# Kernel tuning notes

Measured on AMD Instinct MI355X. Metric: run time of the kernel, lower is better.

## Reference

```python
import jax, jax.numpy as jnp
import numpy as np

N_NODES = 10000
N_EDGES = 320000
HIDDEN = 16
LABELS = 7


def setup_inputs() -> dict:
    key = jax.random.key(0)
    k1, k2, k3, k4, k5 = jax.random.split(key, 5)
    features = jax.random.normal(k1, (N_NODES, N_NODES), dtype=jnp.float32)
    src = jax.random.randint(k2, (N_EDGES,), 0, N_NODES, dtype=jnp.int64)
    dst = jax.random.randint(k3, (N_EDGES,), 0, N_NODES, dtype=jnp.int64)
    # Glorot-ish params as in DGL GraphConv
    W1 = jax.random.normal(k4, (N_NODES, HIDDEN), dtype=jnp.float32) * (1.0 / np.sqrt(N_NODES))
    b1 = jnp.zeros((HIDDEN,), dtype=jnp.float32)
    W2 = jax.random.normal(k5, (HIDDEN, LABELS), dtype=jnp.float32) * (1.0 / np.sqrt(HIDDEN))
    b2 = jnp.zeros((LABELS,), dtype=jnp.float32)
    return {"features": features, "src": src, "dst": dst,
            "W1": W1, "b1": b1, "W2": W2, "b2": b2}


def reference(features, src, dst, W1, b1, W2, b2):
    N = features.shape[0]
    ones = jnp.ones(src.shape[0], dtype=features.dtype)
    out_deg = jnp.clip(jax.ops.segment_sum(ones, src, num_segments=N), 1.0)
    in_deg = jnp.clip(jax.ops.segment_sum(ones, dst, num_segments=N), 1.0)
    norm_src = jax.lax.rsqrt(out_deg)[:, None]  # D_out^{-1/2}
    norm_dst = jax.lax.rsqrt(in_deg)[:, None]   # D_in^{-1/2}

    def gconv(h, W, b):
        # DGL GraphConv norm='both'; in_feats >= out_feats so W applied first
        h = (h * norm_src) @ W                       # [N, out]
        agg = jax.ops.segment_sum(h[src], dst, num_segments=N)
        return agg * norm_dst + b

    h = jax.nn.relu(gconv(features, W1, b1))  # relu(relu(.)) == relu(.)
    return gconv(h, W2, b2)
```

## Files before the change

kernel.cpp:

```cpp
#include <hip/hip_runtime.h>


constexpr int NN  = 10000;
constexpr int NE  = 320000;
constexpr int HID = 16;
constexpr int LAB = 7;
constexpr int CAP = 128;

__global__ void k_count_fill(const int* __restrict__ src, const int* __restrict__ dst,
                             int* __restrict__ cnt_out, int* __restrict__ cnt_in,
                             int* __restrict__ esrc) {
  const int e = blockIdx.x * blockDim.x + threadIdx.x;
  if (e < NE) {
    const int s = src[e], d = dst[e];
    atomicAdd(&cnt_out[s], 1);
    const int p = atomicAdd(&cnt_in[d], 1);
    if (p < CAP) esrc[(d << 7) + p] = s;
  }
}

__global__ __launch_bounds__(256) void k_gemm1(const float* __restrict__ F,
                                               const float* __restrict__ W1,
                                               const int* __restrict__ cnt_out,
                                               float* __restrict__ Y1a,
                                               float* __restrict__ Y1b) {
  constexpr int BJ = 500;
  constexpr int TILES = 10;
  __shared__ float wT[HID * BJ];
  const int tid  = threadIdx.x;
  const int lane = tid & 63;
  const int wave = tid >> 6;
  const int row0 = blockIdx.x * 16 + wave * 4;
  const int jbase = blockIdx.y * 5000;
  float* __restrict__ Yout = blockIdx.y ? Y1b : Y1a;

  float acc[4][HID];
  #pragma unroll
  for (int m = 0; m < 4; ++m)
    #pragma unroll
    for (int k = 0; k < HID; ++k) acc[m][k] = 0.0f;

  for (int t = 0; t < TILES; ++t) {
    const int jt = jbase + t * BJ;
    __syncthreads();
    for (int u = tid; u < BJ * 4; u += 256) {
      const int j = u >> 2, k4 = u & 3;
      const float4 v = *(const float4*)(W1 + (size_t)(jt + j) * HID + k4 * 4);
      wT[(k4 * 4 + 0) * BJ + j] = v.x;
      wT[(k4 * 4 + 1) * BJ + j] = v.y;
      wT[(k4 * 4 + 2) * BJ + j] = v.z;
      wT[(k4 * 4 + 3) * BJ + j] = v.w;
    }
    __syncthreads();

    const float* Fr = F + (size_t)row0 * NN + jt;
    #pragma unroll
    for (int c = 0; c < 2; ++c) {
      const int j4 = lane + 64 * c;
      if (j4 < BJ / 4) {
        const int j = j4 * 4;
        const float4 f0 = *(const float4*)(Fr + j);
        const float4 f1 = *(const float4*)(Fr + NN + j);
        const float4 f2 = *(const float4*)(Fr + 2 * NN + j);
        const float4 f3 = *(const float4*)(Fr + 3 * NN + j);
        #pragma unroll
        for (int k = 0; k < HID; ++k) {
          const float4 w = *(const float4*)(wT + k * BJ + j);
          acc[0][k] = fmaf(f0.x, w.x, fmaf(f0.y, w.y, fmaf(f0.z, w.z, fmaf(f0.w, w.w, acc[0][k]))));
          acc[1][k] = fmaf(f1.x, w.x, fmaf(f1.y, w.y, fmaf(f1.z, w.z, fmaf(f1.w, w.w, acc[1][k]))));
          acc[2][k] = fmaf(f2.x, w.x, fmaf(f2.y, w.y, fmaf(f2.z, w.z, fmaf(f2.w, w.w, acc[2][k]))));
          acc[3][k] = fmaf(f3.x, w.x, fmaf(f3.y, w.y, fmaf(f3.z, w.z, fmaf(f3.w, w.w, acc[3][k]))));
        }
      }
    }
  }

  #pragma unroll
  for (int m = 0; m < 4; ++m)
    #pragma unroll
    for (int k = 0; k < HID; ++k) {
      float v = acc[m][k];
      #pragma unroll
      for (int off = 32; off > 0; off >>= 1) v += __shfl_down(v, off, 64);
      acc[m][k] = v;
    }

  if (lane == 0) {
    #pragma unroll
    for (int m = 0; m < 4; ++m) {
      const int row = row0 + m;
      const float s = rsqrtf(fmaxf((float)cnt_out[row], 1.0f));
      float4 o0 = {acc[m][0] * s, acc[m][1] * s, acc[m][2] * s, acc[m][3] * s};
      float4 o1 = {acc[m][4] * s, acc[m][5] * s, acc[m][6] * s, acc[m][7] * s};
      float4 o2 = {acc[m][8] * s, acc[m][9] * s, acc[m][10] * s, acc[m][11] * s};
      float4 o3 = {acc[m][12] * s, acc[m][13] * s, acc[m][14] * s, acc[m][15] * s};
      float4* yp = (float4*)(Yout + (size_t)row * HID);
      yp[0] = o0; yp[1] = o1; yp[2] = o2; yp[3] = o3;
    }
  }
}

__global__ __launch_bounds__(256) void k_gather1(
    const int* __restrict__ cnt_out, const int* __restrict__ cnt_in,
    const int* __restrict__ esrc,
    const float* __restrict__ Y1a, const float* __restrict__ Y1b,
    const float* __restrict__ b1, const float* __restrict__ W2,
    float* __restrict__ H2) {
  __shared__ float hsh[4][16];
  const int tid = threadIdx.x, lane = tid & 63, wave = tid >> 6;
  const int i = blockIdx.x * 4 + wave;
  const int n = min(cnt_in[i], CAP);
  const int* el = esrc + ((size_t)i << 7);
  const int sub = lane >> 4, k = lane & 15;
  float sum = 0.0f;
  for (int e = sub; e < n; e += 4) {
    const int s = el[e];
    sum += Y1a[s * HID + k] + Y1b[s * HID + k];
  }
  sum += __shfl_down(sum, 32, 64);
  sum += __shfl_down(sum, 16, 64);
  if (lane < 16) {
    const float ndv = rsqrtf(fmaxf((float)n, 1.0f));
    hsh[wave][k] = fmaxf(fmaf(sum, ndv, b1[k]), 0.0f);
  }
  __syncthreads();
  if (lane < 8) {
    float z = 0.0f;
    if (lane < LAB) {
      #pragma unroll
      for (int kk = 0; kk < HID; ++kk)
        z = fmaf(hsh[wave][kk], W2[kk * LAB + lane], z);
      z *= rsqrtf(fmaxf((float)cnt_out[i], 1.0f));
    }
    H2[i * 8 + lane] = z;
  }
}

__global__ __launch_bounds__(256) void k_gather2(
    const int* __restrict__ cnt_in, const int* __restrict__ esrc,
    const float* __restrict__ H2, const float* __restrict__ b2,
    float* __restrict__ out) {
  const int tid = threadIdx.x, lane = tid & 63, wave = tid >> 6;
  const int i = blockIdx.x * 4 + wave;
  const int n = min(cnt_in[i], CAP);
  const int* el = esrc + ((size_t)i << 7);
  const int sub = lane >> 3, c = lane & 7;
  float sum = 0.0f;
  for (int e = sub; e < n; e += 8) {
    sum += H2[(el[e] << 3) + c];
  }
  sum += __shfl_down(sum, 32, 64);
  sum += __shfl_down(sum, 16, 64);
  sum += __shfl_down(sum, 8, 64);
  if (lane < LAB) {
    const float ndv = rsqrtf(fmaxf((float)n, 1.0f));
    out[i * LAB + lane] = fmaf(sum, ndv, b2[lane]);
  }
}

extern "C" void kernel_launch(void* const* d_in, const int* in_sizes, int n_in,
                              void* d_out, int out_size, void* d_ws, size_t ws_size,
                              hipStream_t stream) {
  const float* F   = (const float*)d_in[0];
  const int*   src = (const int*)d_in[1];
  const int*   dst = (const int*)d_in[2];
  const float* W1  = (const float*)d_in[3];
  const float* b1  = (const float*)d_in[4];
  const float* W2  = (const float*)d_in[5];
  const float* b2  = (const float*)d_in[6];
  float* out = (float*)d_out;

  int* cnt_out = (int*)d_ws;
  int* cnt_in  = cnt_out + NN;
  int* esrc    = cnt_in + NN;
  float* Y1a   = (float*)(esrc + NN * CAP);
  float* Y1b   = Y1a + NN * HID;
  float* H2    = Y1b + NN * HID;

  hipMemsetAsync(d_ws, 0, 2 * NN * sizeof(int), stream);
  k_count_fill<<<(NE + 255) / 256, 256, 0, stream>>>(src, dst, cnt_out, cnt_in, esrc);
  k_gemm1<<<dim3(625, 2), 256, 0, stream>>>(F, W1, cnt_out, Y1a, Y1b);
  k_gather1<<<NN / 4, 256, 0, stream>>>(cnt_out, cnt_in, esrc, Y1a, Y1b, b1, W2, H2);
  k_gather2<<<NN / 4, 256, 0, stream>>>(cnt_in, esrc, H2, b2, out);
}
```

Baseline: 628.4 us.

## Split GEMM1 K-dimension into ten segments with persistent blocks and butterfly reduction

Restructures the 10000x10000 by 16 GEMM so each block holds a 1000-column slice of W1 in LDS once, then loops over many row groups, writing per-segment partial sums. A separate kernel reduces the ten partials and applies the out-degree scaling. A transposing butterfly shuffle reduction replaces the per-accumulator full reductions. This removes repeated W1 tile reloads and lowers reduction cost, at the price of an extra partial buffer, an extra kernel, and a 512-thread block whose 64-float accumulator array adds register pressure. The degree normalisation now uses the uncapped in-degree, and gather1 computes the layer-2 projection with shuffles instead of shared memory.

```diff
diff --git a/kernel.cpp b/kernel.cpp
--- a/kernel.cpp
+++ b/kernel.cpp
@@ -1,11 +1,16 @@
 #include <hip/hip_runtime.h>
 
 
-constexpr int NN  = 10000;
-constexpr int NE  = 320000;
-constexpr int HID = 16;
-constexpr int LAB = 7;
-constexpr int CAP = 128;
+constexpr int NN    = 10000;
+constexpr int NE    = 320000;
+constexpr int HID   = 16;
+constexpr int LAB   = 7;
+constexpr int CAP   = 128;
+constexpr int SEG   = 1000;
+constexpr int SEGF4 = SEG / 4;
+constexpr int NSEG  = NN / SEG;
+constexpr int GX    = 50;
+constexpr int WPS   = GX * 8;
 
 __global__ void k_count_fill(const int* __restrict__ src, const int* __restrict__ dst,
                              int* __restrict__ cnt_out, int* __restrict__ cnt_in,
@@ -19,121 +24,191 @@
   }
 }
 
-__global__ __launch_bounds__(256) void k_gemm1(const float* __restrict__ F,
-                                               const float* __restrict__ W1,
-                                               const int* __restrict__ cnt_out,
-                                               float* __restrict__ Y1a,
-                                               float* __restrict__ Y1b) {
-  constexpr int BJ = 500;
-  constexpr int TILES = 10;
-  __shared__ float wT[HID * BJ];
+__global__ __launch_bounds__(512, 4) void k_gemm1(const float* __restrict__ F,
+                                                  const float* __restrict__ W1,
+                                                  float* __restrict__ Y1p) {
+  __shared__ float wT[HID * SEG];
   const int tid  = threadIdx.x;
   const int lane = tid & 63;
   const int wave = tid >> 6;
-  const int row0 = blockIdx.x * 16 + wave * 4;
-  const int jbase = blockIdx.y * 5000;
-  float* __restrict__ Yout = blockIdx.y ? Y1b : Y1a;
-
-  float acc[4][HID];
+  const int seg  = blockIdx.y;
+  const int j0   = seg * SEG;
+
+  for (int u = tid; u < SEG * 4; u += 512) {
+    const int j = u >> 2, k4 = u & 3;
+    const float4 v = *(const float4*)(W1 + (size_t)(j0 + j) * HID + k4 * 4);
+    wT[(k4 * 4 + 0) * SEG + j] = v.x;
+    wT[(k4 * 4 + 1) * SEG + j] = v.y;
+    wT[(k4 * 4 + 2) * SEG + j] = v.z;
+    wT[(k4 * 4 + 3) * SEG + j] = v.w;
+  }
+  __syncthreads();
+
+  const int wg = blockIdx.x * 8 + wave;
+  float* __restrict__ Yo = Y1p + (size_t)seg * NN * HID;
+  const float4* __restrict__ F4 = (const float4*)F;
+  const int cols0 = j0 >> 2;
+  constexpr int RS = NN / 4;
+
+  for (int round = 0; round < 6; ++round) {
+    const int r0 = (wg + round * WPS) * 4;
+    float a[64];
+    #pragma unroll
+    for (int v = 0; v < 64; ++v) a[v] = 0.0f;
+    const size_t b0 = (size_t)r0 * RS + cols0;
+
+    auto do_c = [&](int j4) {
+      const float4 f0 = F4[b0 + j4];
+      const float4 f1 = F4[b0 + RS + j4];
+      const float4 f2 = F4[b0 + 2 * RS + j4];
+      const float4 f3 = F4[b0 + 3 * RS + j4];
+      #pragma unroll
+      for (int k = 0; k < HID; ++k) {
+        const float4 w = *(const float4*)(wT + k * SEG + (j4 << 2));
+        a[k]      = fmaf(f0.x, w.x, fmaf(f0.y, w.y, fmaf(f0.z, w.z, fmaf(f0.w, w.w, a[k]))));
+        a[16 + k] = fmaf(f1.x, w.x, fmaf(f1.y, w.y, fmaf(f1.z, w.z, fmaf(f1.w, w.w, a[16 + k]))));
+        a[32 + k] = fmaf(f2.x, w.x, fmaf(f2.y, w.y, fmaf(f2.z, w.z, fmaf(f2.w, w.w, a[32 + k]))));
+        a[48 + k] = fmaf(f3.x, w.x, fmaf(f3.y, w.y, fmaf(f3.z, w.z, fmaf(f3.w, w.w, a[48 + k]))));
+      }
+    };
+    #pragma unroll
+    for (int c = 0; c < 3; ++c) do_c(c * 64 + lane);
+    { const int j4 = 192 + lane; if (j4 < SEGF4) do_c(j4); }
+
+    #pragma unroll
+    for (int i = 0; i < 32; ++i) {
+      const float s0 = (lane & 32) ? a[i] : a[i + 32];
+      const float r  = __shfl_xor(s0, 32, 64);
+      a[i] = ((lane & 32) ? a[i + 32] : a[i]) + r;
+    }
+    #pragma unroll
+    for (int i = 0; i < 16; ++i) {
+      const float s0 = (lane & 16) ? a[i] : a[i + 16];
+      const float r  = __shfl_xor(s0, 16, 64);
+      a[i] = ((lane & 16) ? a[i + 16] : a[i]) + r;
+    }
+    #pragma unroll
+    for (int i = 0; i < 8; ++i) {
+      const float s0 = (lane & 8) ? a[i] : a[i + 8];
+      const float r  = __shfl_xor(s0, 8, 64);
+      a[i] = ((lane & 8) ? a[i + 8] : a[i]) + r;
+    }
+    #pragma unroll
+    for (int i = 0; i < 4; ++i) {
+      const float s0 = (lane & 4) ? a[i] : a[i + 4];
+      const float r  = __shfl_xor(s0, 4, 64);
+      a[i] = ((lane & 4) ? a[i + 4] : a[i]) + r;
+    }
+    #pragma unroll
+    for (int i = 0; i < 2; ++i) {
+      const float s0 = (lane & 2) ? a[i] : a[i + 2];
+      const float r  = __shfl_xor(s0, 2, 64);
+      a[i] = ((lane & 2) ? a[i + 2] : a[i]) + r;
+    }
+    {
+      const float s0 = (lane & 1) ? a[0] : a[1];
+      const float r  = __shfl_xor(s0, 1, 64);
+      a[0] = ((lane & 1) ? a[1] : a[0]) + r;
+    }
+    Yo[(size_t)r0 * HID + lane] = a[0];
+  }
+
+  {
+    const int row = 9600 + wg;
+    float a2[16];
+    #pragma unroll
+    for (int k = 0; k < 16; ++k) a2[k] = 0.0f;
+    const size_t b0 = (size_t)row * RS + cols0;
+
+    auto do_ct = [&](int j4) {
+      const float4 f0 = F4[b0 + j4];
+      #pragma unroll
+      for (int k = 0; k < HID; ++k) {
+        const float4 w = *(const float4*)(wT + k * SEG + (j4 << 2));
+        a2[k] = fmaf(f0.x, w.x, fmaf(f0.y, w.y, fmaf(f0.z, w.z, fmaf(f0.w, w.w, a2[k]))));
+      }
+    };
+    #pragma unroll
+    for (int c = 0; c < 3; ++c) do_ct(c * 64 + lane);
+    { const int j4 = 192 + lane; if (j4 < SEGF4) do_ct(j4); }
+
+    #pragma unroll
+    for (int k = 0; k < 16; ++k) {
+      a2[k] += __shfl_xor(a2[k], 32, 64);
+      a2[k] += __shfl_xor(a2[k], 16, 64);
+    }
+    #pragma unroll
+    for (int i = 0; i < 8; ++i) {
+      const float s0 = (lane & 8) ? a2[i] : a2[i + 8];
+      const float r  = __shfl_xor(s0, 8, 64);
+      a2[i] = ((lane & 8) ? a2[i + 8] : a2[i]) + r;
+    }
+    #pragma unroll
+    for (int i = 0; i < 4; ++i) {
+      const float s0 = (lane & 4) ? a2[i] : a2[i + 4];
+      const float r  = __shfl_xor(s0, 4, 64);
+      a2[i] = ((lane & 4) ? a2[i + 4] : a2[i]) + r;
+    }
+    #pragma unroll
+    for (int i = 0; i < 2; ++i) {
+      const float s0 = (lane & 2) ? a2[i] : a2[i + 2];
+      const float r  = __shfl_xor(s0, 2, 64);
+      a2[i] = ((lane & 2) ? a2[i + 2] : a2[i]) + r;
+    }
+    {
+      const float s0 = (lane & 1) ? a2[0] : a2[1];
+      const float r  = __shfl_xor(s0, 1, 64);
+      a2[0] = ((lane & 1) ? a2[1] : a2[0]) + r;
+    }
+    if (lane < 16) Yo[(size_t)row * HID + lane] = a2[0];
+  }
+}
+
+__global__ __launch_bounds__(256) void k_scale_reduce(const float* __restrict__ Y1p,
+                                                      const int* __restrict__ cnt_out,
+                                                      float* __restrict__ Y1) {
+  const int t = blockIdx.x * 256 + threadIdx.x;
+  if (t >= NN * HID / 4) return;
+  const float4* __restrict__ P = (const float4*)Y1p;
+  float4 s = P[t];
   #pragma unroll
-  for (int m = 0; m < 4; ++m)
-    #pragma unroll
-    for (int k = 0; k < HID; ++k) acc[m][k] = 0.0f;
-
-  for (int t = 0; t < TILES; ++t) {
-    const int jt = jbase + t * BJ;
-    __syncthreads();
-    for (int u = tid; u < BJ * 4; u += 256) {
-      const int j = u >> 2, k4 = u & 3;
-      const float4 v = *(const float4*)(W1 + (size_t)(jt + j) * HID + k4 * 4);
-      wT[(k4 * 4 + 0) * BJ + j] = v.x;
-      wT[(k4 * 4 + 1) * BJ + j] = v.y;
-      wT[(k4 * 4 + 2) * BJ + j] = v.z;
-      wT[(k4 * 4 + 3) * BJ + j] = v.w;
-    }
-    __syncthreads();
-
-    const float* Fr = F + (size_t)row0 * NN + jt;
-    #pragma unroll
-    for (int c = 0; c < 2; ++c) {
-      const int j4 = lane + 64 * c;
-      if (j4 < BJ / 4) {
-        const int j = j4 * 4;
-        const float4 f0 = *(const float4*)(Fr + j);
-        const float4 f1 = *(const float4*)(Fr + NN + j);
-        const float4 f2 = *(const float4*)(Fr + 2 * NN + j);
-        const float4 f3 = *(const float4*)(Fr + 3 * NN + j);
-        #pragma unroll
-        for (int k = 0; k < HID; ++k) {
-          const float4 w = *(const float4*)(wT + k * BJ + j);
-          acc[0][k] = fmaf(f0.x, w.x, fmaf(f0.y, w.y, fmaf(f0.z, w.z, fmaf(f0.w, w.w, acc[0][k]))));
-          acc[1][k] = fmaf(f1.x, w.x, fmaf(f1.y, w.y, fmaf(f1.z, w.z, fmaf(f1.w, w.w, acc[1][k]))));
-          acc[2][k] = fmaf(f2.x, w.x, fmaf(f2.y, w.y, fmaf(f2.z, w.z, fmaf(f2.w, w.w, acc[2][k]))));
-          acc[3][k] = fmaf(f3.x, w.x, fmaf(f3.y, w.y, fmaf(f3.z, w.z, fmaf(f3.w, w.w, acc[3][k]))));
-        }
-      }
-    }
-  }
-
-  #pragma unroll
-  for (int m = 0; m < 4; ++m)
-    #pragma unroll
-    for (int k = 0; k < HID; ++k) {
-      float v = acc[m][k];
-      #pragma unroll
-      for (int off = 32; off > 0; off >>= 1) v += __shfl_down(v, off, 64);
-      acc[m][k] = v;
-    }
-
-  if (lane == 0) {
-    #pragma unroll
-    for (int m = 0; m < 4; ++m) {
-      const int row = row0 + m;
-      const float s = rsqrtf(fmaxf((float)cnt_out[row], 1.0f));
-      float4 o0 = {acc[m][0] * s, acc[m][1] * s, acc[m][2] * s, acc[m][3] * s};
-      float4 o1 = {acc[m][4] * s, acc[m][5] * s, acc[m][6] * s, acc[m][7] * s};
-      float4 o2 = {acc[m][8] * s, acc[m][9] * s, acc[m][10] * s, acc[m][11] * s};
-      float4 o3 = {acc[m][12] * s, acc[m][13] * s, acc[m][14] * s, acc[m][15] * s};
-      float4* yp = (float4*)(Yout + (size_t)row * HID);
-      yp[0] = o0; yp[1] = o1; yp[2] = o2; yp[3] = o3;
-    }
-  }
+  for (int g = 1; g < NSEG; ++g) {
+    const float4 v = P[(size_t)g * (NN * HID / 4) + t];
+    s.x += v.x; s.y += v.y; s.z += v.z; s.w += v.w;
+  }
+  const int row = t >> 2;
+  const float ns = rsqrtf(fmaxf((float)cnt_out[row], 1.0f));
+  s.x *= ns; s.y *= ns; s.z *= ns; s.w *= ns;
+  ((float4*)Y1)[t] = s;
 }
 
 __global__ __launch_bounds__(256) void k_gather1(
     const int* __restrict__ cnt_out, const int* __restrict__ cnt_in,
-    const int* __restrict__ esrc,
-    const float* __restrict__ Y1a, const float* __restrict__ Y1b,
+    const int* __restrict__ esrc, const float* __restrict__ Y1,
     const float* __restrict__ b1, const float* __restrict__ W2,
     float* __restrict__ H2) {
-  __shared__ float hsh[4][16];
   const int tid = threadIdx.x, lane = tid & 63, wave = tid >> 6;
   const int i = blockIdx.x * 4 + wave;
-  const int n = min(cnt_in[i], CAP);
+  const int nin = cnt_in[i];
+  const int n = min(nin, CAP);
   const int* el = esrc + ((size_t)i << 7);
   const int sub = lane >> 4, k = lane & 15;
   float sum = 0.0f;
   for (int e = sub; e < n; e += 4) {
     const int s = el[e];
-    sum += Y1a[s * HID + k] + Y1b[s * HID + k];
+    sum += Y1[s * HID + k];
   }
   sum += __shfl_down(sum, 32, 64);
   sum += __shfl_down(sum, 16, 64);
-  if (lane < 16) {
-    const float ndv = rsqrtf(fmaxf((float)n, 1.0f));
-    hsh[wave][k] = fmaxf(fmaf(sum, ndv, b1[k]), 0.0f);
-  }
-  __syncthreads();
-  if (lane < 8) {
-    float z = 0.0f;
-    if (lane < LAB) {
-      #pragma unroll
-      for (int kk = 0; kk < HID; ++kk)
-        z = fmaf(hsh[wave][kk], W2[kk * LAB + lane], z);
-      z *= rsqrtf(fmaxf((float)cnt_out[i], 1.0f));
-    }
-    H2[i * 8 + lane] = z;
-  }
+  const float ndv = rsqrtf(fmaxf((float)nin, 1.0f));
+  const float h = fmaxf(fmaf(sum, ndv, b1[k]), 0.0f);
+  const int c = (lane < LAB) ? lane : 0;
+  float z = 0.0f;
+  #pragma unroll
+  for (int kk = 0; kk < HID; ++kk)
+    z = fmaf(__shfl(h, kk, 64), W2[kk * LAB + c], z);
+  z *= rsqrtf(fmaxf((float)cnt_out[i], 1.0f));
+  if (lane < 8) H2[i * 8 + lane] = (lane < LAB) ? z : 0.0f;
 }
 
 __global__ __launch_bounds__(256) void k_gather2(
@@ -142,7 +217,8 @@
     float* __restrict__ out) {
   const int tid = threadIdx.x, lane = tid & 63, wave = tid >> 6;
   const int i = blockIdx.x * 4 + wave;
-  const int n = min(cnt_in[i], CAP);
+  const int nin = cnt_in[i];
+  const int n = min(nin, CAP);
   const int* el = esrc + ((size_t)i << 7);
   const int sub = lane >> 3, c = lane & 7;
   float sum = 0.0f;
@@ -153,7 +229,7 @@
   sum += __shfl_down(sum, 16, 64);
   sum += __shfl_down(sum, 8, 64);
   if (lane < LAB) {
-    const float ndv = rsqrtf(fmaxf((float)n, 1.0f));
+    const float ndv = rsqrtf(fmaxf((float)nin, 1.0f));
     out[i * LAB + lane] = fmaf(sum, ndv, b2[lane]);
   }
 }
@@ -173,13 +249,14 @@
   int* cnt_out = (int*)d_ws;
   int* cnt_in  = cnt_out + NN;
   int* esrc    = cnt_in + NN;
-  float* Y1a   = (float*)(esrc + NN * CAP);
-  float* Y1b   = Y1a + NN * HID;
-  float* H2    = Y1b + NN * HID;
+  float* Y1p   = (float*)(esrc + (size_t)NN * CAP);
+  float* Y1    = Y1p + (size_t)NSEG * NN * HID;
+  float* H2    = Y1 + (size_t)NN * HID;
 
   hipMemsetAsync(d_ws, 0, 2 * NN * sizeof(int), stream);
   k_count_fill<<<(NE + 255) / 256, 256, 0, stream>>>(src, dst, cnt_out, cnt_in, esrc);
-  k_gemm1<<<dim3(625, 2), 256, 0, stream>>>(F, W1, cnt_out, Y1a, Y1b);
-  k_gather1<<<NN / 4, 256, 0, stream>>>(cnt_out, cnt_in, esrc, Y1a, Y1b, b1, W2, H2);
+  k_gemm1<<<dim3(GX, NSEG), 512, 0, stream>>>(F, W1, Y1p);
+  k_scale_reduce<<<(NN * HID / 4 + 255) / 256, 256, 0, stream>>>(Y1p, cnt_out, Y1);
+  k_gather1<<<NN / 4, 256, 0, stream>>>(cnt_out, cnt_in, esrc, Y1, b1, W2, H2);
   k_gather2<<<NN / 4, 256, 0, stream>>>(cnt_in, esrc, H2, b2, out);
 }
```

New measurement: 1.174 ms. +86.8%, slower.
